# Optimization experiments

Measured on AMD Instinct MI355X. Metric: run time of the kernel, lower is better.

Reference implementation:

```python
import jax, jax.numpy as jnp
import numpy as np

D_MODEL, D_STATE, D_CONV, EXPAND = 128, 4, 2, 2
D_INNER = EXPAND * D_MODEL            # 256
DT_RANK = (D_MODEL + 15) // 16        # 8
B, L = 4096, 45


def setup_inputs() -> dict:
    key = jax.random.key(0)
    ks = jax.random.split(key, 10)
    s = lambda k, shp, sc=0.02: jax.random.normal(k, shp, dtype=jnp.float32) * sc
    inp = {
        "ConcatEmbedding": jax.random.normal(ks[0], (B, L, D_MODEL), dtype=jnp.float32),
        "pad_mask": jax.random.randint(ks[1], (B, L), 0, 2, dtype=jnp.int32),
        "W_in": s(ks[2], (2 * D_INNER, D_MODEL)),
        "conv_w": s(ks[3], (D_INNER, D_CONV), 0.5),
        "conv_b": jnp.zeros((D_INNER,), jnp.float32),
        "W_x": s(ks[4], (DT_RANK + 2 * D_STATE, D_INNER)),
        "W_dt": s(ks[5], (D_INNER, DT_RANK), 0.1),
        "b_dt": jnp.full((D_INNER,), -2.0, jnp.float32),  # softplus(-2) ~ 0.127
        "A_log": jnp.log(jnp.tile(jnp.arange(1, D_STATE + 1, dtype=jnp.float32), (D_INNER, 1))),
        "D": jnp.ones((D_INNER,), jnp.float32),
        "W_out": s(ks[6], (D_MODEL, D_INNER)),
    }
    return inp


def _mamba(x, W_in, conv_w, conv_b, W_x, W_dt, b_dt, A_log, D, W_out):
    Bn, Ln, _ = x.shape
    xz = jnp.einsum('bld,ed->ble', x, W_in)          # (B,L,2*D_INNER)
    xc, z = jnp.split(xz, 2, axis=-1)
    # causal depthwise conv1d, kernel D_CONV, pad left D_CONV-1
    xp = jnp.pad(xc, ((0, 0), (D_CONV - 1, 0), (0, 0)))
    xconv = conv_b
    for k in range(D_CONV):  # tiny fixed loop (2 taps)
        xconv = xconv + xp[:, k:k + Ln] * conv_w[:, k]
    u = jax.nn.silu(xconv)                            # (B,L,E)
    x_dbl = jnp.einsum('ble,re->blr', u, W_x)
    dt = x_dbl[..., :DT_RANK]
    Bm = x_dbl[..., DT_RANK:DT_RANK + D_STATE]        # (B,L,N)
    Cm = x_dbl[..., DT_RANK + D_STATE:]               # (B,L,N)
    delta = jax.nn.softplus(jnp.einsum('blr,er->ble', dt, W_dt) + b_dt)  # (B,L,E)
    A = -jnp.exp(A_log)                               # (E,N)
    dA = jnp.exp(delta[..., None] * A)                # (B,L,E,N)
    dBu = delta[..., None] * Bm[:, :, None, :] * u[..., None]

    def step(h, inp):
        dA_t, dBu_t, C_t = inp
        h = dA_t * h + dBu_t                          # (B,E,N)
        y = jnp.einsum('ben,bn->be', h, C_t)
        return h, y

    h0 = jnp.zeros((Bn, D_INNER, D_STATE), x.dtype)
    xs = (dA.transpose(1, 0, 2, 3), dBu.transpose(1, 0, 2, 3), Cm.transpose(1, 0, 2))
    _, ys = jax.lax.scan(step, h0, xs)
    y = ys.transpose(1, 0, 2) + u * D                 # (B,L,E)
    y = y * jax.nn.silu(z)
    return jnp.einsum('ble,de->bld', y, W_out)


def reference(ConcatEmbedding, pad_mask, W_in, conv_w, conv_b, W_x, W_dt, b_dt, A_log, D, W_out):
    feat = _mamba(ConcatEmbedding, W_in, conv_w, conv_b, W_x, W_dt, b_dt, A_log, D, W_out)
    coff = 1.0 - pad_mask.astype(jnp.float32)         # (B,L)
    rep = jnp.sum(coff[:, :, None] * feat, axis=1) / jnp.sum(coff, axis=1)[:, None]
    return rep, feat
```

## Files before the change

kernel.cpp:

```cpp
#include <hip/hip_runtime.h>

#define NB 4096
#define LSEQ 45
#define DM 128
#define DI 256
#define SAUG 264
#define SX   136
#define MR 48

typedef __attribute__((ext_vector_type(8))) _Float16 f16x8;
typedef __attribute__((ext_vector_type(4))) _Float16 f16x4;
typedef __attribute__((ext_vector_type(4))) float f32x4;

#define WS_WP   0
#define WS_WZ   65536
#define WS_WX   98304
#define WS_WO   102400
#define WS_TOT  135168

__global__ void convert_weights(const float* __restrict__ W_in,
                                const float* __restrict__ conv_w,
                                const float* __restrict__ W_x,
                                const float* __restrict__ W_out,
                                _Float16* __restrict__ ws) {
    int i = blockIdx.x * 256 + threadIdx.x;
    if (i < 65536) {
        int e = i >> 8, k = i & 255;
        float w = (k < 128) ? conv_w[2*e + 1] * W_in[e*128 + k]
                            : conv_w[2*e]     * W_in[e*128 + k - 128];
        ws[i] = (_Float16)w;
    } else if (i < 98304) {
        int j = i - 65536;
        ws[i] = (_Float16)W_in[(256 + (j >> 7))*128 + (j & 127)];
    } else if (i < 102400) {
        ws[i] = (_Float16)W_x[i - 98304];
    } else if (i < WS_TOT) {
        ws[i] = (_Float16)W_out[i - 102400];
    }
}

__device__ __forceinline__ float fast_silu(float v) {
    return v * __builtin_amdgcn_rcpf(1.f + __expf(-v));
}

__global__ __launch_bounds__(256, 4)
void mamba_mfma_kernel(const float* __restrict__ x,
                       const int*   __restrict__ pad_mask,
                       const float* __restrict__ conv_b,
                       const float* __restrict__ W_dt,
                       const float* __restrict__ b_dt,
                       const float* __restrict__ A_log,
                       const float* __restrict__ Dvec,
                       const _Float16* __restrict__ ws,
                       float* __restrict__ out)
{
    const int b = blockIdx.x;
    const int t = threadIdx.x;
    const int lane = t & 63;
    const int wv = t >> 6;
    const int ar = lane & 15;
    const int kg = lane >> 4;

    __shared__ __align__(16) unsigned char pool[40880];
    _Float16* s_u  = (_Float16*)pool;
    _Float16* s_x  = (_Float16*)(pool + 25344);
    _Float16* s_dt = (_Float16*)(pool + 38672);
    float*    s_bc = (float*)(pool + 39440);

    for (int i = t; i < 4*17; i += 256) {
        const int rr = i / 17, c = i % 17;
        const int row = (rr == 0) ? 0 : 45 + rr;
        ((f32x4*)(s_x + row*SX))[c] = f32x4{0.f,0.f,0.f,0.f};
    }
    const float* xb = x + (size_t)b * LSEQ * DM;
    for (int idx = t; idx < LSEQ * 32; idx += 256) {
        const int row = idx >> 5;
        const int c4 = (idx & 31) << 2;
        const float4 v = *(const float4*)(xb + row*DM + c4);
        f16x4 h; h.x = (_Float16)v.x; h.y = (_Float16)v.y;
        h.z = (_Float16)v.z; h.w = (_Float16)v.w;
        *(f16x4*)(s_x + (row+1)*SX + c4) = h;
    }
    if (t < LSEQ)
        *(float*)(s_x + (t+1)*SX + 128) = 1.0f - (float)pad_mask[b*LSEQ + t];
    __syncthreads();
    if (t == 0) {
        float cs = 0.f;
        for (int l = 0; l < LSEQ; ++l) cs += *(const float*)(s_x + (l+1)*SX + 128);
        *(float*)(s_x + 128) = __builtin_amdgcn_rcpf(cs);
    }

    {
        f32x4 acc[4][3];
        #pragma unroll
        for (int j = 0; j < 4; ++j)
            #pragma unroll
            for (int m = 0; m < 3; ++m) acc[j][m] = f32x4{0.f,0.f,0.f,0.f};
        const _Float16* Wp = ws + WS_WP;
        #pragma unroll
        for (int ks = 0; ks < 8; ++ks) {
            f16x8 afr[3];
            #pragma unroll
            for (int m = 0; m < 3; ++m) {
                const int row = m*16 + ar;
                afr[m] = (ks < 4)
                    ? *(const f16x8*)(s_x + (row+1)*SX + ks*32 + kg*8)
                    : *(const f16x8*)(s_x + row*SX + (ks-4)*32 + kg*8);
            }
            #pragma unroll
            for (int j = 0; j < 4; ++j) {
                const int e = (wv*4 + j)*16 + ar;
                f16x8 bfr = *(const f16x8*)(Wp + e*256 + ks*32 + kg*8);
                #pragma unroll
                for (int m = 0; m < 3; ++m)
                    acc[j][m] = __builtin_amdgcn_mfma_f32_16x16x32_f16(afr[m], bfr, acc[j][m], 0, 0, 0);
            }
        }
        #pragma unroll
        for (int j = 0; j < 4; ++j) {
            const int e = (wv*4 + j)*16 + ar;
            const float cbe = conv_b[e];
            #pragma unroll
            for (int m = 0; m < 3; ++m)
                #pragma unroll
                for (int i = 0; i < 4; ++i) {
                    const int row = m*16 + kg*4 + i;
                    s_u[row*SAUG + e] = (_Float16)fast_silu(acc[j][m][i] + cbe);
                }
        }
    }
    __syncthreads();

    if (wv < 3) {
        f32x4 acc = f32x4{0.f,0.f,0.f,0.f};
        const _Float16* Wxp = ws + WS_WX;
        #pragma unroll
        for (int ks = 0; ks < 8; ++ks) {
            f16x8 afr = *(const f16x8*)(s_u + (wv*16 + ar)*SAUG + ks*32 + kg*8);
            f16x8 bfr = *(const f16x8*)(Wxp + ar*256 + ks*32 + kg*8);
            acc = __builtin_amdgcn_mfma_f32_16x16x32_f16(afr, bfr, acc, 0, 0, 0);
        }
        #pragma unroll
        for (int i = 0; i < 4; ++i) {
            const int row = wv*16 + kg*4 + i;
            if (ar < 8) s_dt[row*8 + ar] = (_Float16)acc[i];
            else if (row < LSEQ) s_bc[row*8 + (ar - 8)] = acc[i];
        }
    }
    __syncthreads();

    {
        const int e = t;
        const float4 wdtA = *(const float4*)(W_dt + e*8);
        const float4 wdtB = *(const float4*)(W_dt + e*8 + 4);
        const float bdt = b_dt[e];
        float Av[4];
        #pragma unroll
        for (int n = 0; n < 4; ++n) Av[n] = -__expf(A_log[e*4 + n]);
        const float Dv = Dvec[e];
        float h0 = 0.f, h1 = 0.f, h2 = 0.f, h3 = 0.f;
        for (int l = 0; l < LSEQ; ++l) {
            const f16x8 dt8 = *(const f16x8*)(s_dt + l*8);
            float dtv = bdt;
            dtv += (float)dt8[0]*wdtA.x + (float)dt8[1]*wdtA.y
                 + (float)dt8[2]*wdtA.z + (float)dt8[3]*wdtA.w;
            dtv += (float)dt8[4]*wdtB.x + (float)dt8[5]*wdtB.y
                 + (float)dt8[6]*wdtB.z + (float)dt8[7]*wdtB.w;
            const float delta = fmaxf(dtv, 0.f) + __logf(1.f + __expf(-fabsf(dtv)));
            const f32x4 xB = *(const f32x4*)(s_bc + l*8);
            const f32x4 xC = *(const f32x4*)(s_bc + l*8 + 4);
            const float ue = (float)s_u[l*SAUG + e];
            const float du = delta * ue;
            h0 = __expf(delta*Av[0])*h0 + du*xB[0];
            h1 = __expf(delta*Av[1])*h1 + du*xB[1];
            h2 = __expf(delta*Av[2])*h2 + du*xB[2];
            h3 = __expf(delta*Av[3])*h3 + du*xB[3];
            const float y = h0*xC[0] + h1*xC[1] + h2*xC[2] + h3*xC[3] + ue*Dv;
            s_u[l*SAUG + e] = (_Float16)y;
        }
    }
    __syncthreads();

    {
        f32x4 acc[4][3];
        #pragma unroll
        for (int j = 0; j < 4; ++j)
            #pragma unroll
            for (int m = 0; m < 3; ++m) acc[j][m] = f32x4{0.f,0.f,0.f,0.f};
        const _Float16* Wzp = ws + WS_WZ;
        #pragma unroll
        for (int ks = 0; ks < 4; ++ks) {
            f16x8 afr[3];
            #pragma unroll
            for (int m = 0; m < 3; ++m)
                afr[m] = *(const f16x8*)(s_x + (m*16 + ar + 1)*SX + ks*32 + kg*8);
            #pragma unroll
            for (int j = 0; j < 4; ++j) {
                const int e = (wv*4 + j)*16 + ar;
                f16x8 bfr = *(const f16x8*)(Wzp + e*128 + ks*32 + kg*8);
                #pragma unroll
                for (int m = 0; m < 3; ++m)
                    acc[j][m] = __builtin_amdgcn_mfma_f32_16x16x32_f16(afr[m], bfr, acc[j][m], 0, 0, 0);
            }
        }
        #pragma unroll
        for (int j = 0; j < 4; ++j) {
            const int e = (wv*4 + j)*16 + ar;
            #pragma unroll
            for (int m = 0; m < 3; ++m)
                #pragma unroll
                for (int i = 0; i < 4; ++i) {
                    const int row = m*16 + kg*4 + i;
                    const float yv = (float)s_u[row*SAUG + e];
                    s_u[row*SAUG + e] = (_Float16)(yv * fast_silu(acc[j][m][i]));
                }
        }
    }
    __syncthreads();

    {
        f32x4 acc[2][3];
        #pragma unroll
        for (int jn = 0; jn < 2; ++jn)
            #pragma unroll
            for (int m = 0; m < 3; ++m) acc[jn][m] = f32x4{0.f,0.f,0.f,0.f};
        const _Float16* Wop = ws + WS_WO;
        #pragma unroll
        for (int ks = 0; ks < 8; ++ks) {
            f16x8 afr[3];
            #pragma unroll
            for (int m = 0; m < 3; ++m)
                afr[m] = *(const f16x8*)(s_u + (m*16 + ar)*SAUG + ks*32 + kg*8);
            #pragma unroll
            for (int jn = 0; jn < 2; ++jn) {
                const int d0 = (wv*2 + jn)*16 + ar;
                f16x8 bfr = *(const f16x8*)(Wop + d0*256 + ks*32 + kg*8);
                #pragma unroll
                for (int m = 0; m < 3; ++m)
                    acc[jn][m] = __builtin_amdgcn_mfma_f32_16x16x32_f16(afr[m], bfr, acc[jn][m], 0, 0, 0);
            }
        }
        float* featb = out + (size_t)NB*DM + (size_t)b*LSEQ*DM;
        float arep[2] = {0.f, 0.f};
        #pragma unroll
        for (int m = 0; m < 3; ++m)
            #pragma unroll
            for (int i = 0; i < 4; ++i) {
                const int row = m*16 + kg*4 + i;
                if (row < LSEQ) {
                    const float cf = *(const float*)(s_x + (row+1)*SX + 128);
                    #pragma unroll
                    for (int jn = 0; jn < 2; ++jn) {
                        const int col = (wv*2 + jn)*16 + ar;
                        const float v = acc[jn][m][i];
                        featb[row*DM + col] = v;
                        arep[jn] += cf * v;
                    }
                }
            }
        const float inv = *(const float*)(s_x + 128);
        #pragma unroll
        for (int jn = 0; jn < 2; ++jn) {
            float r = arep[jn];
            r += __shfl_xor(r, 16);
            r += __shfl_xor(r, 32);
            if (kg == 0)
                out[(size_t)b*DM + (wv*2 + jn)*16 + ar] = r * inv;
        }
    }
}

extern "C" void kernel_launch(void* const* d_in, const int* in_sizes, int n_in,
                              void* d_out, int out_size, void* d_ws, size_t ws_size,
                              hipStream_t stream) {
    const float* x        = (const float*)d_in[0];
    const int*   pad_mask = (const int*)d_in[1];
    const float* W_in     = (const float*)d_in[2];
    const float* conv_w   = (const float*)d_in[3];
    const float* conv_b   = (const float*)d_in[4];
    const float* W_x      = (const float*)d_in[5];
    const float* W_dt     = (const float*)d_in[6];
    const float* b_dt     = (const float*)d_in[7];
    const float* A_log    = (const float*)d_in[8];
    const float* Dvec     = (const float*)d_in[9];
    const float* W_out    = (const float*)d_in[10];
    _Float16* ws = (_Float16*)d_ws;

    convert_weights<<<(WS_TOT + 255)/256, 256, 0, stream>>>(W_in, conv_w, W_x, W_out, ws);
    mamba_mfma_kernel<<<NB, 256, 0, stream>>>(x, pad_mask, conv_b, W_dt, b_dt,
                                              A_log, Dvec, ws, (float*)d_out);
}
```

Before: 187.1 us.

## Load x fragments directly from global memory, drop LDS staging, raise occupancy

Removes the shared-memory staging buffer for the fp16 input tile. MFMA A-fragments are now loaded straight from global fp32 x and converted in registers, with row clamping and zeroing for the causal shift. This shrinks LDS use and removes a barrier, so launch bounds rise from 4 to 5 blocks per CU. W_dt is pre-converted to fp16 and the dt projection uses fdot2. The cost is that x is re-read from global (or cache) in both the conv GEMM and the z GEMM, and the per-fragment loads are uncoalesced.

New measurement: 305.6 us. 63.4% more time.

```diff
diff --git a/kernel.cpp b/kernel.cpp
--- a/kernel.cpp
+++ b/kernel.cpp
@@ -5,23 +5,24 @@
 #define DM 128
 #define DI 256
 #define SAUG 264
-#define SX   136
 #define MR 48
 
 typedef __attribute__((ext_vector_type(8))) _Float16 f16x8;
-typedef __attribute__((ext_vector_type(4))) _Float16 f16x4;
+typedef __attribute__((ext_vector_type(2))) _Float16 f16x2;
 typedef __attribute__((ext_vector_type(4))) float f32x4;
 
 #define WS_WP   0
 #define WS_WZ   65536
 #define WS_WX   98304
 #define WS_WO   102400
-#define WS_TOT  135168
+#define WS_WDT  135168
+#define WS_TOT  137216
 
 __global__ void convert_weights(const float* __restrict__ W_in,
                                 const float* __restrict__ conv_w,
                                 const float* __restrict__ W_x,
                                 const float* __restrict__ W_out,
+                                const float* __restrict__ W_dt,
                                 _Float16* __restrict__ ws) {
     int i = blockIdx.x * 256 + threadIdx.x;
     if (i < 65536) {
@@ -34,8 +35,10 @@
         ws[i] = (_Float16)W_in[(256 + (j >> 7))*128 + (j & 127)];
     } else if (i < 102400) {
         ws[i] = (_Float16)W_x[i - 98304];
+    } else if (i < 135168) {
+        ws[i] = (_Float16)W_out[i - 102400];
     } else if (i < WS_TOT) {
-        ws[i] = (_Float16)W_out[i - 102400];
+        ws[i] = (_Float16)W_dt[i - 135168];
     }
 }
 
@@ -43,11 +46,23 @@
     return v * __builtin_amdgcn_rcpf(1.f + __expf(-v));
 }
 
-__global__ __launch_bounds__(256, 4)
+__device__ __forceinline__ f16x8 ldcvt(const float* __restrict__ p) {
+    const float4 a = *(const float4*)p;
+    const float4 b = *(const float4*)(p + 4);
+    auto p0 = __builtin_amdgcn_cvt_pkrtz(a.x, a.y);
+    auto p1 = __builtin_amdgcn_cvt_pkrtz(a.z, a.w);
+    auto p2 = __builtin_amdgcn_cvt_pkrtz(b.x, b.y);
+    auto p3 = __builtin_amdgcn_cvt_pkrtz(b.z, b.w);
+    f16x8 r;
+    r[0] = p0[0]; r[1] = p0[1]; r[2] = p1[0]; r[3] = p1[1];
+    r[4] = p2[0]; r[5] = p2[1]; r[6] = p3[0]; r[7] = p3[1];
+    return r;
+}
+
+__global__ __launch_bounds__(256, 5)
 void mamba_mfma_kernel(const float* __restrict__ x,
                        const int*   __restrict__ pad_mask,
                        const float* __restrict__ conv_b,
-                       const float* __restrict__ W_dt,
                        const float* __restrict__ b_dt,
                        const float* __restrict__ A_log,
                        const float* __restrict__ Dvec,
@@ -61,34 +76,16 @@
     const int ar = lane & 15;
     const int kg = lane >> 4;
 
-    __shared__ __align__(16) unsigned char pool[40880];
-    _Float16* s_u  = (_Float16*)pool;
-    _Float16* s_x  = (_Float16*)(pool + 25344);
-    _Float16* s_dt = (_Float16*)(pool + 38672);
-    float*    s_bc = (float*)(pool + 39440);
-
-    for (int i = t; i < 4*17; i += 256) {
-        const int rr = i / 17, c = i % 17;
-        const int row = (rr == 0) ? 0 : 45 + rr;
-        ((f32x4*)(s_x + row*SX))[c] = f32x4{0.f,0.f,0.f,0.f};
-    }
+    __shared__ __align__(16) unsigned char pool[27760];
+    _Float16* s_u    = (_Float16*)pool;
+    _Float16* s_dt   = (_Float16*)(pool + 25344);
+    float*    s_bc   = (float*)(pool + 26112);
+    float*    s_coff = (float*)(pool + 27552);
+    float*    s_inv  = (float*)(pool + 27744);
+
     const float* xb = x + (size_t)b * LSEQ * DM;
-    for (int idx = t; idx < LSEQ * 32; idx += 256) {
-        const int row = idx >> 5;
-        const int c4 = (idx & 31) << 2;
-        const float4 v = *(const float4*)(xb + row*DM + c4);
-        f16x4 h; h.x = (_Float16)v.x; h.y = (_Float16)v.y;
-        h.z = (_Float16)v.z; h.w = (_Float16)v.w;
-        *(f16x4*)(s_x + (row+1)*SX + c4) = h;
-    }
-    if (t < LSEQ)
-        *(float*)(s_x + (t+1)*SX + 128) = 1.0f - (float)pad_mask[b*LSEQ + t];
-    __syncthreads();
-    if (t == 0) {
-        float cs = 0.f;
-        for (int l = 0; l < LSEQ; ++l) cs += *(const float*)(s_x + (l+1)*SX + 128);
-        *(float*)(s_x + 128) = __builtin_amdgcn_rcpf(cs);
-    }
+    if (t < MR)
+        s_coff[t] = (t < LSEQ) ? 1.0f - (float)pad_mask[b*LSEQ + t] : 0.f;
 
     {
         f32x4 acc[4][3];
@@ -103,9 +100,15 @@
             #pragma unroll
             for (int m = 0; m < 3; ++m) {
                 const int row = m*16 + ar;
-                afr[m] = (ks < 4)
-                    ? *(const f16x8*)(s_x + (row+1)*SX + ks*32 + kg*8)
-                    : *(const f16x8*)(s_x + row*SX + (ks-4)*32 + kg*8);
+                if (ks < 4) {
+                    const int rc = (row < LSEQ) ? row : LSEQ-1;
+                    afr[m] = ldcvt(xb + rc*DM + ks*32 + kg*8);
+                } else {
+                    int rm = row - 1;
+                    rm = (rm < 0) ? 0 : ((rm < LSEQ) ? rm : LSEQ-1);
+                    afr[m] = ldcvt(xb + rm*DM + (ks-4)*32 + kg*8);
+                    if (m == 0 && row == 0) afr[m] = f16x8{0,0,0,0,0,0,0,0};
+                }
             }
             #pragma unroll
             for (int j = 0; j < 4; ++j) {
@@ -131,6 +134,12 @@
     }
     __syncthreads();
 
+    if (t == 0) {
+        float cs = 0.f;
+        for (int l = 0; l < LSEQ; ++l) cs += s_coff[l];
+        s_inv[0] = __builtin_amdgcn_rcpf(cs);
+    }
+
     if (wv < 3) {
         f32x4 acc = f32x4{0.f,0.f,0.f,0.f};
         const _Float16* Wxp = ws + WS_WX;
@@ -151,21 +160,30 @@
 
     {
         const int e = t;
-        const float4 wdtA = *(const float4*)(W_dt + e*8);
-        const float4 wdtB = *(const float4*)(W_dt + e*8 + 4);
+        const f16x8 wdt8 = *(const f16x8*)(ws + WS_WDT + e*8);
         const float bdt = b_dt[e];
         float Av[4];
         #pragma unroll
         for (int n = 0; n < 4; ++n) Av[n] = -__expf(A_log[e*4 + n]);
         const float Dv = Dvec[e];
+#if __has_builtin(__builtin_amdgcn_fdot2)
+        f16x2 w0 = f16x2{wdt8[0], wdt8[1]}, w1 = f16x2{wdt8[2], wdt8[3]};
+        f16x2 w2 = f16x2{wdt8[4], wdt8[5]}, w3 = f16x2{wdt8[6], wdt8[7]};
+#endif
         float h0 = 0.f, h1 = 0.f, h2 = 0.f, h3 = 0.f;
         for (int l = 0; l < LSEQ; ++l) {
             const f16x8 dt8 = *(const f16x8*)(s_dt + l*8);
             float dtv = bdt;
-            dtv += (float)dt8[0]*wdtA.x + (float)dt8[1]*wdtA.y
-                 + (float)dt8[2]*wdtA.z + (float)dt8[3]*wdtA.w;
-            dtv += (float)dt8[4]*wdtB.x + (float)dt8[5]*wdtB.y
-                 + (float)dt8[6]*wdtB.z + (float)dt8[7]*wdtB.w;
+#if __has_builtin(__builtin_amdgcn_fdot2)
+            dtv = __builtin_amdgcn_fdot2(f16x2{dt8[0], dt8[1]}, w0, dtv, false);
+            dtv = __builtin_amdgcn_fdot2(f16x2{dt8[2], dt8[3]}, w1, dtv, false);
+            dtv = __builtin_amdgcn_fdot2(f16x2{dt8[4], dt8[5]}, w2, dtv, false);
+            dtv = __builtin_amdgcn_fdot2(f16x2{dt8[6], dt8[7]}, w3, dtv, false);
+#else
+            #pragma unroll
+            for (int r = 0; r < 8; ++r)
+                dtv += (float)dt8[r] * (float)wdt8[r];
+#endif
             const float delta = fmaxf(dtv, 0.f) + __logf(1.f + __expf(-fabsf(dtv)));
             const f32x4 xB = *(const f32x4*)(s_bc + l*8);
             const f32x4 xC = *(const f32x4*)(s_bc + l*8 + 4);
@@ -192,8 +210,11 @@
         for (int ks = 0; ks < 4; ++ks) {
             f16x8 afr[3];
             #pragma unroll
-            for (int m = 0; m < 3; ++m)
-                afr[m] = *(const f16x8*)(s_x + (m*16 + ar + 1)*SX + ks*32 + kg*8);
+            for (int m = 0; m < 3; ++m) {
+                const int row = m*16 + ar;
+                const int rc = (row < LSEQ) ? row : LSEQ-1;
+                afr[m] = ldcvt(xb + rc*DM + ks*32 + kg*8);
+            }
             #pragma unroll
             for (int j = 0; j < 4; ++j) {
                 const int e = (wv*4 + j)*16 + ar;
@@ -248,7 +269,7 @@
             for (int i = 0; i < 4; ++i) {
                 const int row = m*16 + kg*4 + i;
                 if (row < LSEQ) {
-                    const float cf = *(const float*)(s_x + (row+1)*SX + 128);
+                    const float cf = s_coff[row];
                     #pragma unroll
                     for (int jn = 0; jn < 2; ++jn) {
                         const int col = (wv*2 + jn)*16 + ar;
@@ -258,7 +279,7 @@
                     }
                 }
             }
-        const float inv = *(const float*)(s_x + 128);
+        const float inv = s_inv[0];
         #pragma unroll
         for (int jn = 0; jn < 2; ++jn) {
             float r = arep[jn];
@@ -286,7 +307,7 @@
     const float* W_out    = (const float*)d_in[10];
     _Float16* ws = (_Float16*)d_ws;
 
-    convert_weights<<<(WS_TOT + 255)/256, 256, 0, stream>>>(W_in, conv_w, W_x, W_out, ws);
-    mamba_mfma_kernel<<<NB, 256, 0, stream>>>(x, pad_mask, conv_b, W_dt, b_dt,
+    convert_weights<<<(WS_TOT + 255)/256, 256, 0, stream>>>(W_in, conv_w, W_x, W_out, W_dt, ws);
+    mamba_mfma_kernel<<<NB, 256, 0, stream>>>(x, pad_mask, conv_b, b_dt,
                                               A_log, Dvec, ws, (float*)d_out);
 }
```
